# Optimization experiments

Measured on AMD Instinct MI355X. Metric: run time of the kernel, lower is better.

## Reference

```python
import jax, jax.numpy as jnp
import numpy as np
import math

CH = 96      # channels
WS = 8       # window size
SS = WS // 2 # stride
NH = 4       # heads
RED = 16     # SE reduction
B, H, W = 2, 128, 128
SCALE = (CH // NH) ** -0.5
LN_EPS = 1e-5


def setup_inputs() -> dict:
    key = jax.random.key(0)
    ks = jax.random.split(key, 16)
    def n(k, shape, s=0.02):
        return jax.random.normal(k, shape, jnp.float32) * s
    gc = CH // 3
    gcr = max(gc // RED, 1)
    return dict(
        low=jax.random.normal(ks[0], (B, CH, H, W), jnp.float32),
        high=jax.random.normal(ks[1], (B, CH, H, W), jnp.float32),
        ln1_g=jnp.ones((CH,), jnp.float32), ln1_b=jnp.zeros((CH,), jnp.float32),
        ln2_g=jnp.ones((CH,), jnp.float32), ln2_b=jnp.zeros((CH,), jnp.float32),
        se_w1=n(ks[2], (3, gcr, gc)), se_w2=n(ks[3], (3, gc, gcr)),
        wq_l=n(ks[4], (CH, CH)), wk_h=n(ks[5], (CH, CH)), wv_h=n(ks[6], (CH, CH)),
        wq_h=n(ks[7], (CH, CH)), wk_l=n(ks[8], (CH, CH)), wv_l=n(ks[9], (CH, CH)),
        wproj_l=n(ks[10], (CH, CH)), wproj_h=n(ks[11], (CH, CH)),
        mlp_w1=n(ks[12], (4 * CH, CH)), mlp_b1=jnp.zeros((4 * CH,), jnp.float32),
        mlp_w2=n(ks[13], (CH, 4 * CH)), mlp_b2=jnp.zeros((CH,), jnp.float32),
    )


def _ln(x, g, b):
    # LayerNorm over channel dim of NCHW tensor
    mu = jnp.mean(x, axis=1, keepdims=True)
    v = jnp.mean((x - mu) ** 2, axis=1, keepdims=True)
    return (x - mu) * jax.lax.rsqrt(v + LN_EPS) * g[None, :, None, None] + b[None, :, None, None]


def _win(low, high, se_w1, se_w2, wq_l, wk_h, wv_h, wq_h, wk_l, wv_l, wp_l, wp_h):
    Bz, C, Hh, Ww = low.shape
    n_h = 0 if Hh <= WS else math.ceil((Hh - WS) / SS)
    n_w = 0 if Ww <= WS else math.ceil((Ww - WS) / SS)
    Hp, Wp = n_h * SS + WS, n_w * SS + WS
    low_p = jnp.pad(low, ((0, 0), (0, 0), (0, Hp - Hh), (0, Wp - Ww)))
    high_p = jnp.pad(high, ((0, 0), (0, 0), (0, Hp - Hh), (0, Wp - Ww)))
    # SE on 3 channel groups of high
    gc = C // 3
    groups = []
    for i in range(3):
        hg = high_p[:, i * gc:(i + 1) * gc]
        pool = hg.mean((2, 3))                        # (B, gc)
        z = jax.nn.relu(pool @ se_w1[i].T)            # (B, gcr)
        s = jax.nn.sigmoid(z @ se_w2[i].T)            # (B, gc)
        groups.append(hg * s[:, :, None, None])
    high_d = jnp.concatenate(groups, axis=1)
    nHw, nWw = n_h + 1, n_w + 1
    idx_h = np.arange(nHw)[:, None] * SS + np.arange(WS)[None, :]  # (nHw, WS)
    idx_w = np.arange(nWw)[:, None] * SS + np.arange(WS)[None, :]  # (nWw, WS)

    def extract(x):  # unfold -> (B*L, C, WS*WS)
        p = x[:, :, idx_h][:, :, :, :, idx_w]          # (B,C,nHw,WS,nWw,WS)
        p = p.transpose(0, 2, 4, 1, 3, 5)              # (B,nHw,nWw,C,WS,WS)
        return p.reshape(Bz * nHw * nWw, C, WS * WS)

    lw, hw = extract(low_p), extract(high_d)
    d = C // NH

    def proj(w, x):  # 1x1 conv on flattened windows
        return jnp.einsum('oc,xcn->xon', w, x).reshape(-1, NH, d, WS * WS)

    ql, kh, vh = proj(wq_l, lw), proj(wk_h, hw), proj(wv_h, hw)
    qh, kl, vl = proj(wq_h, hw), proj(wk_l, lw), proj(wv_l, lw)
    a_lh = jax.nn.softmax(jnp.einsum('xhdn,xhdm->xhnm', ql, kh) * SCALE, axis=-1)
    a_hl = jax.nn.softmax(jnp.einsum('xhdn,xhdm->xhnm', qh, kl) * SCALE, axis=-1)
    ol = jnp.einsum('xhnm,xhdm->xhdn', a_lh, vh).reshape(Bz, nHw, nWw, C, WS, WS)
    oh = jnp.einsum('xhnm,xhdm->xhdn', a_hl, vl).reshape(Bz, nHw, nWw, C, WS, WS)
    ih = idx_h[:, :, None, None]
    iw = idx_w[None, None, :, :]

    def fold(p):  # scatter-add overlapping windows back
        p = p.transpose(0, 3, 1, 4, 2, 5)              # (B,C,nHw,WS,nWw,WS)
        return jnp.zeros((Bz, C, Hp, Wp), p.dtype).at[:, :, ih, iw].add(p)

    cnt = jnp.zeros((Hp, Wp), jnp.float32).at[ih, iw].add(jnp.ones((nHw, WS, nWw, WS), jnp.float32))
    out_l = (fold(ol) / cnt)[:, :, :Hh, :Ww]
    out_h = (fold(oh) / cnt)[:, :, :Hh, :Ww]
    return (low + jnp.einsum('oc,bchw->bohw', wp_l, out_l),
            high + jnp.einsum('oc,bchw->bohw', wp_h, out_h))


def reference(low, high, ln1_g, ln1_b, ln2_g, ln2_b, se_w1, se_w2,
              wq_l, wk_h, wv_h, wq_h, wk_l, wv_l, wproj_l, wproj_h,
              mlp_w1, mlp_b1, mlp_w2, mlp_b2):
    wargs = (se_w1, se_w2, wq_l, wk_h, wv_h, wq_h, wk_l, wv_l, wproj_l, wproj_h)
    l1 = _ln(low, ln1_g, ln1_b)
    h1 = _ln(high, ln1_g, ln1_b)
    o1_l, o1_h = _win(l1, h1, *wargs)
    low1 = low + o1_l
    high1 = high + o1_h
    s = SS
    ls = jnp.roll(low1, (-s, -s), (2, 3))
    hs = jnp.roll(high1, (-s, -s), (2, 3))
    o2_l, o2_h = _win(_ln(ls, ln2_g, ln2_b), _ln(hs, ln2_g, ln2_b), *wargs)
    low2 = low1 + jnp.roll(o2_l, (s, s), (2, 3))
    high2 = high1 + jnp.roll(o2_h, (s, s), (2, 3))

    def mlp(x):
        xf = x.transpose(0, 2, 3, 1)  # B,H,W,C
        h = jax.nn.gelu(xf @ mlp_w1.T + mlp_b1, approximate=False)
        return (h @ mlp_w2.T + mlp_b2).transpose(0, 3, 1, 2)

    return (low2 + mlp(low2), high2 + mlp(high2))
```

## Files before the change

### kernel.cpp

```cpp
#include <hip/hip_runtime.h>
#include <math.h>

#define CHN 96
#define HW 16384
#define NWIN 31
#define SCALE_F 0.20412414523193154f

typedef __attribute__((ext_vector_type(8))) __bf16 bf16x8;
typedef __attribute__((ext_vector_type(4))) float f32x4;
typedef __attribute__((ext_vector_type(8))) unsigned short u16x8;

__device__ __forceinline__ int rfl(int v) { return __builtin_amdgcn_readfirstlane(v); }

__device__ __forceinline__ unsigned short f2bf(float f) {
  union { float f; unsigned u; } v; v.f = f;
  unsigned r = v.u + 0x7fffu + ((v.u >> 16) & 1u);
  return (unsigned short)(r >> 16);
}
__device__ __forceinline__ float bf2f(unsigned short h) {
  union { unsigned u; float f; } v; v.u = ((unsigned)h) << 16;
  return v.f;
}
__device__ __forceinline__ float ldv(const float* p, size_t i) { return p[i]; }
__device__ __forceinline__ float ldv(const unsigned short* p, size_t i) { return bf2f(p[i]); }
__device__ __forceinline__ bf16x8 ld8(const unsigned short* p) {
  return *(const bf16x8*)__builtin_assume_aligned(p, 16);
}
__device__ __forceinline__ u16x8 ld8u(const unsigned short* p) {
  return *(const u16x8*)__builtin_assume_aligned(p, 16);
}
__device__ __forceinline__ bf16x8 zf8() {
  union { unsigned long long u[2]; bf16x8 v; } z;
  z.u[0] = 0ull; z.u[1] = 0ull;
  return z.v;
}
__device__ __forceinline__ void ld8f(const float* p, float* o) {
  float4 a = *(const float4*)__builtin_assume_aligned(p, 16);
  float4 b = *(const float4*)__builtin_assume_aligned(p + 4, 16);
  o[0] = a.x; o[1] = a.y; o[2] = a.z; o[3] = a.w;
  o[4] = b.x; o[5] = b.y; o[6] = b.z; o[7] = b.w;
}
__device__ __forceinline__ void ld8f(const unsigned short* p, float* o) {
  u16x8 v = ld8u(p);
#pragma unroll
  for (int u = 0; u < 8; ++u) o[u] = bf2f(v[u]);
}
__device__ __forceinline__ void ld4f(const float* p, float* o) {
  float4 a = *(const float4*)__builtin_assume_aligned(p, 16);
  o[0] = a.x; o[1] = a.y; o[2] = a.z; o[3] = a.w;
}
__device__ __forceinline__ void ld4f(const unsigned short* p, float* o) {
  ushort4 v = *(const ushort4*)__builtin_assume_aligned(p, 8);
  o[0] = bf2f(v.x); o[1] = bf2f(v.y); o[2] = bf2f(v.z); o[3] = bf2f(v.w);
}

__device__ __forceinline__ float gelu_sig(float x) {
  return x * __builtin_amdgcn_rcpf(1.f + __expf(-1.702f * x));
}

template <typename T>
__global__ __launch_bounds__(256) void ln2_k(const T* __restrict__ xl, const T* __restrict__ xh,
                                             float* __restrict__ mu_l, float* __restrict__ rs_l,
                                             float* __restrict__ mu_h, float* __restrict__ rs_h) {
  int which = blockIdx.x >> 5;
  int idx = (blockIdx.x & 31) * 256 + threadIdx.x;
  int pix0 = idx * 4;
  const T* xt = which ? xh : xl;
  float* mu = which ? mu_h : mu_l;
  float* rstd = which ? rs_h : rs_l;
  int b = pix0 >> 14, p = pix0 & 16383;
  const T* xp = xt + (size_t)b * CHN * HW + p;
  float s[4] = {0.f, 0.f, 0.f, 0.f}, s2[4] = {0.f, 0.f, 0.f, 0.f};
#pragma unroll 8
  for (int c = 0; c < CHN; ++c) {
    float v4[4];
    ld4f(xp + (size_t)c * HW, v4);
#pragma unroll
    for (int j = 0; j < 4; ++j) {
      s[j] += v4[j];
      s2[j] = fmaf(v4[j], v4[j], s2[j]);
    }
  }
  float4 mo, ro;
  float m0 = s[0] * (1.f / 96.f), m1 = s[1] * (1.f / 96.f);
  float m2 = s[2] * (1.f / 96.f), m3 = s[3] * (1.f / 96.f);
  mo.x = m0; mo.y = m1; mo.z = m2; mo.w = m3;
  ro.x = rsqrtf(fmaf(-m0, m0, s2[0] * (1.f / 96.f)) + 1e-5f);
  ro.y = rsqrtf(fmaf(-m1, m1, s2[1] * (1.f / 96.f)) + 1e-5f);
  ro.z = rsqrtf(fmaf(-m2, m2, s2[2] * (1.f / 96.f)) + 1e-5f);
  ro.w = rsqrtf(fmaf(-m3, m3, s2[3] * (1.f / 96.f)) + 1e-5f);
  *(float4*)&mu[pix0] = mo;
  *(float4*)&rstd[pix0] = ro;
}

template <typename T>
__global__ __launch_bounds__(256) void pool_k(const T* __restrict__ x,
                                              const float* __restrict__ mu,
                                              const float* __restrict__ rstd,
                                              const float* __restrict__ g,
                                              const float* __restrict__ bt,
                                              float* __restrict__ pool) {
  int blk = blockIdx.x;
  int b = blk / CHN, c = blk % CHN;
  const T* xp = x + (size_t)(b * CHN + c) * HW;
  const float* mup = mu + b * HW;
  const float* rp = rstd + b * HW;
  int t = threadIdx.x;
  float s = 0.f;
  for (int p0 = t * 4; p0 < HW; p0 += 1024) {
    float v4[4];
    ld4f(xp + p0, v4);
    float4 m4 = *(const float4*)&mup[p0];
    float4 r4 = *(const float4*)&rp[p0];
    s += (v4[0] - m4.x) * r4.x + (v4[1] - m4.y) * r4.y +
         (v4[2] - m4.z) * r4.z + (v4[3] - m4.w) * r4.w;
  }
  __shared__ float red[256];
  red[t] = s;
  __syncthreads();
  for (int k = 128; k > 0; k >>= 1) {
    if (t < k) red[t] += red[t + k];
    __syncthreads();
  }
  if (t == 0) pool[blk] = g[c] * (red[0] * (1.f / 16384.f)) + bt[c];
}

__global__ __launch_bounds__(256) void se_k(const float* __restrict__ pool,
                                            const float* __restrict__ w1,
                                            const float* __restrict__ w2,
                                            float* __restrict__ s_se) {
  int t = threadIdx.x;
  if (t >= 2 * CHN) return;
  int b = t / CHN, c = t % CHN;
  int i = c >> 5, cl = c & 31;
  const float* pg = pool + b * CHN + i * 32;
  const float* w1p = w1 + i * 64;
  float z0 = 0.f, z1 = 0.f;
#pragma unroll 8
  for (int k = 0; k < 32; ++k) {
    float p = pg[k];
    z0 = fmaf(p, w1p[k], z0);
    z1 = fmaf(p, w1p[32 + k], z1);
  }
  z0 = fmaxf(z0, 0.f);
  z1 = fmaxf(z1, 0.f);
  float a = z0 * w2[i * 64 + cl * 2] + z1 * w2[i * 64 + cl * 2 + 1];
  s_se[t] = 1.f / (1.f + __expf(-a));
}

__global__ __launch_bounds__(256) void cvt_k(const float* __restrict__ w1,
                                             const float* __restrict__ w2,
                                             const float* __restrict__ p0,
                                             const float* __restrict__ p1,
                                             const float* __restrict__ p2,
                                             const float* __restrict__ p3,
                                             const float* __restrict__ p4,
                                             const float* __restrict__ p5,
                                             const float* __restrict__ q0,
                                             const float* __restrict__ q1,
                                             unsigned short* __restrict__ w1b,
                                             unsigned short* __restrict__ w2b,
                                             unsigned short* __restrict__ wqb,
                                             unsigned short* __restrict__ wpb) {
  int i = blockIdx.x * 256 + threadIdx.x;
  if (i < 36864) {
    w1b[i] = f2bf(w1[i]);
    w2b[i] = f2bf(w2[i]);
  }
  if (i < 55296) {
    int tt = i / 9216, rem = i - tt * 9216;
    const float* ps[6] = {p0, p1, p2, p3, p4, p5};
    wqb[i] = f2bf(ps[tt][rem]);
  }
  if (i < 18432) {
    wpb[i] = f2bf(i < 9216 ? q0[i] : q1[i - 9216]);
  }
}

template <typename T>
__global__ __launch_bounds__(256, 3) void proj_k(
    const T* __restrict__ lowp, const T* __restrict__ highp,
    const float* __restrict__ mu_l, const float* __restrict__ rs_l,
    const float* __restrict__ mu_h, const float* __restrict__ rs_h,
    const float* __restrict__ g, const float* __restrict__ bt,
    const float* __restrict__ s_se,
    const unsigned short* __restrict__ wqb,
    unsigned short* __restrict__ qkv) {
  __shared__ __align__(16) unsigned short sh[13312];
  unsigned short* Xl = sh;
  unsigned short* Xh = sh + 6656;
  int t = threadIdx.x;
  int lane = t & 63;
  int w = rfl(t >> 6);
  int n16 = lane & 15, quad = lane >> 4;
  int tile = blockIdx.x;
  int Pb = tile * 64;
  int b = Pb >> 14, rr0 = Pb & 16383;

  {
    int pg = t & 7;
    float mul8[8], rsl8[8], muh8[8], rsh8[8];
    ld8f(mu_l + (size_t)b * HW + rr0 + pg * 8, mul8);
    ld8f(rs_l + (size_t)b * HW + rr0 + pg * 8, rsl8);
    ld8f(mu_h + (size_t)b * HW + rr0 + pg * 8, muh8);
    ld8f(rs_h + (size_t)b * HW + rr0 + pg * 8, rsh8);
#pragma unroll
    for (int k = 0; k < 3; ++k) {
      int c = (t + k * 256) >> 3;
      float gc = g[c], bc = bt[c], sc = s_se[b * CHN + c];
      float xl8[8], xh8[8];
      ld8f(lowp + (size_t)(b * CHN + c) * HW + rr0 + pg * 8, xl8);
      ld8f(highp + (size_t)(b * CHN + c) * HW + rr0 + pg * 8, xh8);
      int cr = c + pg * 8; if (cr >= 96) cr -= 96;
#pragma unroll
      for (int u = 0; u < 8; ++u) {
        int px = pg * 8 + u;
        Xl[px * 104 + cr] = f2bf((xl8[u] - mul8[u]) * rsl8[u] * gc + bc);
        Xh[px * 104 + cr] = f2bf(((xh8[u] - muh8[u]) * rsh8[u] * gc + bc) * sc);
      }
    }
  }
  __syncthreads();

  int tmain = (0x4310 >> (4 * w)) & 15;
  const unsigned short* Xm = (w == 0 || w == 3) ? Xl : Xh;
  const unsigned short* Xv = (w < 2) ? Xh : Xl;
  bf16x8 af[12], av[12];
  int rotb = n16 >> 3;
#pragma unroll
  for (int mi = 0; mi < 4; ++mi)
#pragma unroll
    for (int k = 0; k < 3; ++k) {
      int gidx = k * 4 + quad + 2 * mi + rotb; if (gidx >= 12) gidx -= 12;
      af[mi * 3 + k] = ld8(&Xm[(mi * 16 + n16) * 104 + gidx * 8]);
      av[mi * 3 + k] = ld8(&Xv[(mi * 16 + n16) * 104 + gidx * 8]);
    }
  __syncthreads();

  unsigned short* tw = sh + w * 3328;
#pragma unroll
  for (int half = 0; half < 2; ++half) {
#pragma unroll
    for (int ni = 0; ni < 6; ++ni) {
      f32x4 a0 = {0.f, 0.f, 0.f, 0.f}, a1 = {0.f, 0.f, 0.f, 0.f};
#pragma unroll
      for (int k = 0; k < 3; ++k) {
        bf16x8 bf = ld8(&wqb[((size_t)tmain * 96 + ni * 16 + n16) * 96 + k * 32 + quad * 8]);
        a0 = __builtin_amdgcn_mfma_f32_16x16x32_bf16(af[(half * 2 + 0) * 3 + k], bf, a0, 0, 0, 0);
        a1 = __builtin_amdgcn_mfma_f32_16x16x32_bf16(af[(half * 2 + 1) * 3 + k], bf, a1, 0, 0, 0);
      }
#pragma unroll
      for (int r = 0; r < 4; ++r) {
        tw[(quad * 4 + r) * 104 + ni * 16 + n16] = f2bf(a0[r]);
        tw[(16 + quad * 4 + r) * 104 + ni * 16 + n16] = f2bf(a1[r]);
      }
    }
#pragma unroll
    for (int c6 = 0; c6 < 6; ++c6) {
      int chunk = lane + 64 * c6;
      int pl2 = chunk / 12, kb2 = chunk - pl2 * 12;
      u16x8 v = ld8u(&tw[pl2 * 104 + kb2 * 8]);
      size_t pix = (size_t)rr0 + half * 32 + pl2;
      *(u16x8*)&qkv[((size_t)(tmain * 2 + b) * HW + pix) * 96 + kb2 * 8] = v;
    }
  }

  int tv = (w < 2) ? 2 : 5;
  int nbase = (w & 1) * 3;
#pragma unroll
  for (int jj = 0; jj < 3; ++jj) {
    int ni = nbase + jj;
    f32x4 acc[4];
#pragma unroll
    for (int mi = 0; mi < 4; ++mi) { f32x4 z = {0.f, 0.f, 0.f, 0.f}; acc[mi] = z; }
#pragma unroll
    for (int k = 0; k < 3; ++k) {
      bf16x8 bf = ld8(&wqb[((size_t)tv * 96 + ni * 16 + n16) * 96 + k * 32 + quad * 8]);
#pragma unroll
      for (int mi = 0; mi < 4; ++mi)
        acc[mi] = __builtin_amdgcn_mfma_f32_16x16x32_bf16(av[mi * 3 + k], bf, acc[mi], 0, 0, 0);
    }
    int feat = ni * 16 + n16;
    size_t rowbase = ((size_t)(tv * 2 + b) * CHN + feat) * HW + rr0;
#pragma unroll
    for (int mi = 0; mi < 4; ++mi) {
      ushort4 o4;
      o4.x = f2bf(acc[mi][0]);
      o4.y = f2bf(acc[mi][1]);
      o4.z = f2bf(acc[mi][2]);
      o4.w = f2bf(acc[mi][3]);
      *(ushort4*)&qkv[rowbase + mi * 16 + quad * 4] = o4;
    }
  }
}

__global__ __launch_bounds__(256, 4) void attn_k(
    const unsigned short* __restrict__ qkv,
    unsigned short* __restrict__ Owin, int shift) {
  __shared__ __align__(16) unsigned short shb[17152];
  unsigned short* Vs = shb;
  unsigned short* P32 = shb + 6912;
  unsigned short* Os = shb;

  int bid = blockIdx.x;
  int dir = bid / 1922;
  int rem = bid - dir * 1922;
  int b = rem / 961;
  int win = rem - b * 961;
  int wy = win / NWIN, wx = win % NWIN;
  int t = threadIdx.x;
  int lane = t & 63;
  int h = rfl(t >> 6);
  int n16 = lane & 15, quad = lane >> 4;

  {
    const unsigned short* vbase = qkv + (size_t)((dir * 3 + 2) * 2 + b) * CHN * HW;
    for (int i = t; i < 1536; i += 256) {
      int c = i >> 4, ry = (i >> 1) & 7, hx = i & 1;
      int gy = (wy * 4 + ry + shift) & 127;
      int gx = (wx * 4 + hx * 4 + shift) & 127;
      ushort4 v4 = *(const ushort4*)(vbase + (size_t)c * HW + gy * 128 + gx);
      *(ushort4*)&Vs[c * 72 + ry * 8 + hx * 4] = v4;
    }
  }

  bf16x8 qa[4], kb4[4];
  {
    const unsigned short* qpm = qkv + (size_t)((dir * 3 + 0) * 2 + b) * CHN * HW;
    const unsigned short* kpm = qkv + (size_t)((dir * 3 + 1) * 2 + b) * CHN * HW;
    if (quad < 3) {
#pragma unroll
      for (int ni = 0; ni < 4; ++ni) {
        int n = ni * 16 + n16;
        int gy = (wy * 4 + (n >> 3) + shift) & 127;
        int gx = (wx * 4 + (n & 7) + shift) & 127;
        size_t pix = (size_t)gy * 128 + gx;
        qa[ni] = ld8(&qpm[pix * 96 + h * 24 + quad * 8]);
        kb4[ni] = ld8(&kpm[pix * 96 + h * 24 + quad * 8]);
      }
    } else {
#pragma unroll
      for (int ni = 0; ni < 4; ++ni) { qa[ni] = zf8(); kb4[ni] = zf8(); }
    }
  }
  __syncthreads();

  const int hP = h * (64 * 40);

  f32x4 sa[4][4];
#pragma unroll
  for (int ni = 0; ni < 4; ++ni)
#pragma unroll
    for (int mi = 0; mi < 4; ++mi) {
      f32x4 z = {0.f, 0.f, 0.f, 0.f};
      sa[ni][mi] = __builtin_amdgcn_mfma_f32_16x16x32_bf16(qa[ni], kb4[mi], z, 0, 0, 0);
    }

#pragma unroll
  for (int ni = 0; ni < 4; ++ni)
#pragma unroll
    for (int r = 0; r < 4; ++r) {
      float e0 = __expf(sa[ni][0][r] * SCALE_F);
      float e1 = __expf(sa[ni][1][r] * SCALE_F);
      float e2 = __expf(sa[ni][2][r] * SCALE_F);
      float e3 = __expf(sa[ni][3][r] * SCALE_F);
      float sm = (e0 + e1) + (e2 + e3);
      sm += __shfl_xor(sm, 1);
      sm += __shfl_xor(sm, 2);
      sm += __shfl_xor(sm, 4);
      sm += __shfl_xor(sm, 8);
      float inv = __builtin_amdgcn_rcpf(sm);
      sa[ni][0][r] = e0 * inv;
      sa[ni][1][r] = e1 * inv;
      sa[ni][2][r] = e2 * inv;
      sa[ni][3][r] = e3 * inv;
    }

  f32x4 oa[4][2];
#pragma unroll
  for (int ni = 0; ni < 4; ++ni) {
    f32x4 z = {0.f, 0.f, 0.f, 0.f};
    oa[ni][0] = z; oa[ni][1] = z;
  }
#pragma unroll
  for (int s = 0; s < 2; ++s) {
#pragma unroll
    for (int ni = 0; ni < 4; ++ni)
#pragma unroll
      for (int r = 0; r < 4; ++r) {
#pragma unroll
        for (int mm = 0; mm < 2; ++mm) {
          int mi = s * 2 + mm;
          P32[hP + (ni * 16 + quad * 4 + r) * 40 + mm * 16 + n16] = f2bf(sa[ni][mi][r]);
        }
      }
    bf16x8 pa[4];
#pragma unroll
    for (int ni = 0; ni < 4; ++ni) pa[ni] = ld8(&P32[hP + (ni * 16 + n16) * 40 + quad * 8]);
    bf16x8 vb0 = ld8(&Vs[(h * 24 + n16) * 72 + s * 32 + quad * 8]);
    bf16x8 vb1 = (n16 < 8) ? ld8(&Vs[(h * 24 + 16 + n16) * 72 + s * 32 + quad * 8]) : zf8();
#pragma unroll
    for (int ni = 0; ni < 4; ++ni) {
      oa[ni][0] = __builtin_amdgcn_mfma_f32_16x16x32_bf16(pa[ni], vb0, oa[ni][0], 0, 0, 0);
      oa[ni][1] = __builtin_amdgcn_mfma_f32_16x16x32_bf16(pa[ni], vb1, oa[ni][1], 0, 0, 0);
    }
  }
  __syncthreads();

#pragma unroll
  for (int ni = 0; ni < 4; ++ni)
#pragma unroll
    for (int r = 0; r < 4; ++r) {
      int n = ni * 16 + quad * 4 + r;
      Os[n * 104 + h * 24 + n16] = f2bf(oa[ni][0][r]);
      if (n16 < 8) Os[n * 104 + h * 24 + 16 + n16] = f2bf(oa[ni][1][r]);
    }
  __syncthreads();

  {
    unsigned short* obase = Owin + (size_t)((dir * 2 + b) * 961 + win) * 64 * CHN;
#pragma unroll
    for (int k = 0; k < 3; ++k) {
      int i = t + k * 256;
      int px = i / 12, cb = i - px * 12;
      u16x8 v = ld8u(&Os[px * 104 + cb * 8]);
      *(u16x8*)&obase[px * CHN + cb * 8] = v;
    }
  }
}

template <typename T>
__global__ __launch_bounds__(256) void combine_k(
    const T* __restrict__ base_l, const T* __restrict__ base_h,
    unsigned short* __restrict__ out_l, unsigned short* __restrict__ out_h,
    const unsigned short* __restrict__ Owin,
    float* __restrict__ mu_lp, float* __restrict__ rs_lp,
    float* __restrict__ mu_hp, float* __restrict__ rs_hp,
    const float* __restrict__ g, const float* __restrict__ bt,
    const unsigned short* __restrict__ wpb2, int shift) {
  __shared__ __align__(16) unsigned short sb[96 * 72];
  __shared__ float red[2][4][64];
  unsigned short* at = sb;
  unsigned short* ot = sb;
  int t = threadIdx.x;
  int lane = t & 63;
  int w = rfl(t >> 6);
  int n16 = lane & 15, quad = lane >> 4;
  int sel = blockIdx.x >> 9;
  int tile = blockIdx.x & 511;
  const T* base = sel ? base_h : base_l;
  unsigned short* outp = sel ? out_h : out_l;
  float* mu = sel ? mu_hp : mu_lp;
  float* rstd = sel ? rs_hp : rs_lp;
  const unsigned short* wpb = wpb2 + sel * 9216;

#pragma unroll
  for (int k = 0; k < 3; ++k) {
    int i = t + k * 256;
    int px = i / 12, cb = i - px * 12;
    int Ps = tile * 64 + px;
    int b = Ps >> 14, rem = Ps & 16383;
    int ys = rem >> 7, xs = rem & 127;
    int wyh = ys >> 2, wxh = xs >> 2;
    float acc[8];
#pragma unroll
    for (int u = 0; u < 8; ++u) acc[u] = 0.f;
    for (int dy = 0; dy < 2; ++dy) {
      int wyc = wyh - 1 + dy;
      if ((unsigned)wyc > 30u) continue;
      int py = ys - wyc * 4;
      for (int dx = 0; dx < 2; ++dx) {
        int wxc = wxh - 1 + dx;
        if ((unsigned)wxc > 30u) continue;
        int pxl = xs - wxc * 4;
        size_t o = ((size_t)((sel * 2 + b) * 961 + wyc * 31 + wxc) * 64 + py * 8 + pxl) * CHN + cb * 8;
        u16x8 v = ld8u(&Owin[o]);
#pragma unroll
        for (int u = 0; u < 8; ++u) acc[u] += bf2f(v[u]);
      }
    }
    union { u16x8 v; unsigned short s[8]; } pk;
#pragma unroll
    for (int u = 0; u < 8; ++u) pk.s[u] = f2bf(acc[u]);
    *(u16x8*)&at[px * 104 + cb * 8] = pk.v;
  }
  __syncthreads();

  bf16x8 af[3];
#pragma unroll
  for (int k = 0; k < 3; ++k)
    af[k] = ld8(&at[(w * 16 + n16) * 104 + k * 32 + quad * 8]);

  f32x4 acc6[6];
#pragma unroll
  for (int ni = 0; ni < 6; ++ni) {
    f32x4 z = {0.f, 0.f, 0.f, 0.f};
    acc6[ni] = z;
#pragma unroll
    for (int k = 0; k < 3; ++k) {
      bf16x8 bf = ld8(&wpb[(ni * 16 + n16) * 96 + k * 32 + quad * 8]);
      acc6[ni] = __builtin_amdgcn_mfma_f32_16x16x32_bf16(af[k], bf, acc6[ni], 0, 0, 0);
    }
  }
  __syncthreads();

#pragma unroll
  for (int ni = 0; ni < 6; ++ni)
#pragma unroll
    for (int r = 0; r < 4; ++r)
      ot[(ni * 16 + n16) * 72 + w * 16 + quad * 4 + r] = f2bf(acc6[ni][r]);
  __syncthreads();

  int Ps0 = tile * 64;
  int b = Ps0 >> 14, rem0 = Ps0 & 16383;
  int ys = rem0 >> 7, xs0 = rem0 & 127;
  int yt = (ys + shift) & 127;
  float icy = (ys >= 4 && ys <= 123) ? 0.5f : 1.f;
  int px = t & 63, c0w = t >> 6;
  int xs = xs0 + px;
  int xt = (xs + shift) & 127;
  float icx = (xs >= 4 && xs <= 123) ? 0.5f : 1.f;
  float invc = icy * icx;
  int pt = b * HW + yt * 128 + xt;
  float m = mu[pt], rs = rstd[pt];
  size_t pixoff = (size_t)yt * 128 + xt;
  float s = 0.f, sq = 0.f;
#pragma unroll
  for (int k = 0; k < 24; ++k) {
    int o = c0w + 4 * k;
    size_t gidx = ((size_t)b * CHN + o) * HW + pixoff;
    float bv = ldv(base, gidx);
    float lnv = (bv - m) * rs * g[o] + bt[o];
    float v = bv + lnv + bf2f(ot[o * 72 + px]) * invc;
    outp[gidx] = f2bf(v);
    s += v;
    sq = fmaf(v, v, sq);
  }
  red[0][c0w][px] = s;
  red[1][c0w][px] = sq;
  __syncthreads();
  if (t < 64) {
    int px2 = t;
    float ss = red[0][0][px2] + red[0][1][px2] + red[0][2][px2] + red[0][3][px2];
    float qq = red[1][0][px2] + red[1][1][px2] + red[1][2][px2] + red[1][3][px2];
    int xs2 = xs0 + px2;
    int xt2 = (xs2 + shift) & 127;
    int pt2 = b * HW + yt * 128 + xt2;
    float mm = ss * (1.f / 96.f);
    float var = fmaf(-mm, mm, qq * (1.f / 96.f));
    mu[pt2] = mm;
    rstd[pt2] = rsqrtf(var + 1e-5f);
  }
}

__global__ __launch_bounds__(256, 2) void mlp_k(
    const unsigned short* __restrict__ x_l, const unsigned short* __restrict__ x_h,
    float* __restrict__ outp,
    const unsigned short* __restrict__ w1b, const float* __restrict__ b1,
    const unsigned short* __restrict__ w2b, const float* __restrict__ b2) {
  __shared__ __align__(16) unsigned char smem[51200];
  unsigned short* Xa = (unsigned short*)smem;
  unsigned short* Ha = (unsigned short*)smem;
  float* Ot = (float*)smem;

  int t = threadIdx.x;
  int lane = t & 63;
  int w = rfl(t >> 6);
  int n16 = lane & 15, quad = lane >> 4;
  int sel = blockIdx.x >> 8;
  int tile = blockIdx.x & 255;
  const unsigned short* x = sel ? x_h : x_l;
  float* op = outp + (size_t)sel * (2 * CHN * HW);
  int Pb = tile * 128;
  int b = Pb >> 14, rr0 = Pb & 16383;

  u16x8 xv6[6];
  int cc6[6], pp6[6];
#pragma unroll
  for (int k = 0; k < 6; ++k) {
    int i = t + k * 256;
    cc6[k] = i >> 4; pp6[k] = i & 15;
    xv6[k] = ld8u(&x[((size_t)b * CHN + cc6[k]) * HW + rr0 + pp6[k] * 8]);
  }
  bf16x8 wf[18];
  float b1v6[6];
#pragma unroll
  for (int h2 = 0; h2 < 2; ++h2)
#pragma unroll
    for (int ni = 0; ni < 3; ++ni) {
      int nrow = h2 * 192 + w * 48 + ni * 16 + n16;
#pragma unroll
      for (int kk = 0; kk < 3; ++kk)
        wf[(h2 * 3 + ni) * 3 + kk] = ld8(&w1b[(size_t)nrow * 96 + kk * 32 + quad * 8]);
      b1v6[h2 * 3 + ni] = b1[nrow];
    }
#pragma unroll
  for (int k = 0; k < 6; ++k) {
    int cr = cc6[k] + 8 * pp6[k];
    if (cr >= 96) cr -= 96;
    if (cr >= 96) cr -= 96;
#pragma unroll
    for (int u = 0; u < 8; ++u) Xa[(pp6[k] * 8 + u) * 104 + cr] = xv6[k][u];
  }
  __syncthreads();

  bf16x8 af[24];
  int rotb = n16 >> 3;
#pragma unroll
  for (int mi = 0; mi < 8; ++mi)
#pragma unroll
    for (int k = 0; k < 3; ++k) {
      int gidx = k * 4 + quad + 2 * mi + rotb;
      if (gidx >= 24) gidx -= 24; else if (gidx >= 12) gidx -= 12;
      af[mi * 3 + k] = ld8(&Xa[(mi * 16 + n16) * 104 + gidx * 8]);
    }
  __syncthreads();

  int ph = w & 1, fh = w >> 1;
  f32x4 acc2[4][3];
#pragma unroll
  for (int g2 = 0; g2 < 4; ++g2)
#pragma unroll
    for (int ni = 0; ni < 3; ++ni) { f32x4 z = {0.f, 0.f, 0.f, 0.f}; acc2[g2][ni] = z; }

#pragma unroll
  for (int half = 0; half < 2; ++half) {
#pragma unroll
    for (int ni = 0; ni < 3; ++ni) {
      f32x4 acc[8];
#pragma unroll
      for (int mi = 0; mi < 8; ++mi) { f32x4 z = {0.f, 0.f, 0.f, 0.f}; acc[mi] = z; }
#pragma unroll
      for (int kk = 0; kk < 3; ++kk) {
        bf16x8 bf = wf[(half * 3 + ni) * 3 + kk];
#pragma unroll
        for (int mi = 0; mi < 8; ++mi)
          acc[mi] = __builtin_amdgcn_mfma_f32_16x16x32_bf16(af[mi * 3 + kk], bf, acc[mi], 0, 0, 0);
      }
      int fl = w * 48 + ni * 16 + n16;
      float b1v = b1v6[half * 3 + ni];
#pragma unroll
      for (int mi = 0; mi < 8; ++mi)
#pragma unroll
        for (int r = 0; r < 4; ++r)
          Ha[(mi * 16 + quad * 4 + r) * 200 + fl] = f2bf(gelu_sig(acc[mi][r] + b1v));
    }
    __syncthreads();

#pragma unroll
    for (int kc = 0; kc < 2; ++kc) {
      bf16x8 w2f[9];
#pragma unroll
      for (int kk = 0; kk < 3; ++kk)
#pragma unroll
        for (int ni = 0; ni < 3; ++ni)
          w2f[kk * 3 + ni] = ld8(&w2b[((size_t)(fh * 48 + ni * 16 + n16)) * 384 +
                                      half * 192 + (kc * 3 + kk) * 32 + quad * 8]);
#pragma unroll
      for (int kk = 0; kk < 3; ++kk) {
        int k0 = kc * 3 + kk;
        bf16x8 a2[4];
#pragma unroll
        for (int g2 = 0; g2 < 4; ++g2)
          a2[g2] = ld8(&Ha[((ph * 4 + g2) * 16 + n16) * 200 + k0 * 32 + quad * 8]);
#pragma unroll
        for (int ni = 0; ni < 3; ++ni)
#pragma unroll
          for (int g2 = 0; g2 < 4; ++g2)
            acc2[g2][ni] = __builtin_amdgcn_mfma_f32_16x16x32_bf16(a2[g2], w2f[kk * 3 + ni], acc2[g2][ni], 0, 0, 0);
      }
    }
    __syncthreads();
  }

#pragma unroll
  for (int g2 = 0; g2 < 4; ++g2)
#pragma unroll
    for (int ni = 0; ni < 3; ++ni)
#pragma unroll
      for (int r = 0; r < 4; ++r)
        Ot[(fh * 48 + ni * 16 + n16) * 132 + (ph * 4 + g2) * 16 + quad * 4 + r] = acc2[g2][ni][r];
  __syncthreads();

#pragma unroll
  for (int k = 0; k < 12; ++k) {
    int i = t + k * 256;
    int o = i >> 5, pg = i & 31;
    size_t gbase = ((size_t)b * CHN + o) * HW + rr0 + pg * 4;
    ushort4 xv = *(const ushort4*)&x[gbase];
    float4 ov = *(const float4*)&Ot[o * 132 + pg * 4];
    float bb = b2[o];
    float4 res;
    res.x = bf2f(xv.x) + ov.x + bb;
    res.y = bf2f(xv.y) + ov.y + bb;
    res.z = bf2f(xv.z) + ov.z + bb;
    res.w = bf2f(xv.w) + ov.w + bb;
    *(float4*)&op[gbase] = res;
  }
}

extern "C" void kernel_launch(void* const* d_in, const int* in_sizes, int n_in,
                              void* d_out, int out_size, void* d_ws, size_t ws_size,
                              hipStream_t stream) {
  (void)in_sizes; (void)n_in; (void)out_size; (void)ws_size;
  const float* low   = (const float*)d_in[0];
  const float* high  = (const float*)d_in[1];
  const float* ln1_g = (const float*)d_in[2];
  const float* ln1_b = (const float*)d_in[3];
  const float* ln2_g = (const float*)d_in[4];
  const float* ln2_b = (const float*)d_in[5];
  const float* se_w1 = (const float*)d_in[6];
  const float* se_w2 = (const float*)d_in[7];
  const float* wq_l  = (const float*)d_in[8];
  const float* wk_h  = (const float*)d_in[9];
  const float* wv_h  = (const float*)d_in[10];
  const float* wq_h  = (const float*)d_in[11];
  const float* wk_l  = (const float*)d_in[12];
  const float* wv_l  = (const float*)d_in[13];
  const float* wp_l  = (const float*)d_in[14];
  const float* wp_h  = (const float*)d_in[15];
  const float* mw1   = (const float*)d_in[16];
  const float* mb1   = (const float*)d_in[17];
  const float* mw2   = (const float*)d_in[18];
  const float* mb2   = (const float*)d_in[19];

  float* ws = (float*)d_ws;
  unsigned short* w1b = (unsigned short*)ws;
  unsigned short* w2b = w1b + 36864;
  unsigned short* wqb = w2b + 36864;
  unsigned short* wpb = wqb + 55296;
  float* mu_l  = ws + 73728;
  float* rs_l  = mu_l + 32768;
  float* mu_h  = rs_l + 32768;
  float* rs_h  = mu_h + 32768;
  float* poolb = rs_h + 32768;
  float* s_se  = poolb + 256;
  unsigned short* low1b  = (unsigned short*)(s_se + 256);
  unsigned short* high1b = low1b + 3145728;
  unsigned short* qkv    = high1b + 3145728;
  unsigned short* Owin   = qkv + 18874368;

  cvt_k<<<216, 256, 0, stream>>>(mw1, mw2, wq_l, wk_h, wv_h, wq_h, wk_l, wv_l,
                                 wp_l, wp_h, w1b, w2b, wqb, wpb);

  ln2_k<float><<<64, 256, 0, stream>>>(low, high, mu_l, rs_l, mu_h, rs_h);

  for (int pass = 0; pass < 2; ++pass) {
    const float* g  = pass ? ln2_g : ln1_g;
    const float* bt = pass ? ln2_b : ln1_b;
    int shift = pass ? 4 : 0;

    if (pass == 0) {
      pool_k<float><<<192, 256, 0, stream>>>(high, mu_h, rs_h, g, bt, poolb);
      se_k<<<1, 256, 0, stream>>>(poolb, se_w1, se_w2, s_se);
      proj_k<float><<<512, 256, 0, stream>>>(low, high, mu_l, rs_l, mu_h, rs_h,
                                             g, bt, s_se, wqb, qkv);
      attn_k<<<2 * 1922, 256, 0, stream>>>(qkv, Owin, shift);
      combine_k<float><<<1024, 256, 0, stream>>>(low, high, low1b, high1b, Owin,
                                                 mu_l, rs_l, mu_h, rs_h,
                                                 g, bt, wpb, shift);
    } else {
      pool_k<unsigned short><<<192, 256, 0, stream>>>(high1b, mu_h, rs_h, g, bt, poolb);
      se_k<<<1, 256, 0, stream>>>(poolb, se_w1, se_w2, s_se);
      proj_k<unsigned short><<<512, 256, 0, stream>>>(low1b, high1b, mu_l, rs_l, mu_h, rs_h,
                                                      g, bt, s_se, wqb, qkv);
      attn_k<<<2 * 1922, 256, 0, stream>>>(qkv, Owin, shift);
      combine_k<unsigned short><<<1024, 256, 0, stream>>>(low1b, high1b, low1b, high1b, Owin,
                                                          mu_l, rs_l, mu_h, rs_h,
                                                          g, bt, wpb, shift);
    }
  }
  mlp_k<<<512, 256, 0, stream>>>(low1b, high1b, (float*)d_out, w1b, mb1, w2b, mb2);
}
```

Measured before the change: 335.7 us.

## Defer softmax normalization via MFMA row-sum and shrink P LDS stride

Replaces the per-row softmax shuffle reductions with exp2 of pre-scaled scores, then computes row sums with an extra MFMA against a ones vector and normalizes the PV output afterwards. The P staging buffer stride drops from 40 to 36, which shrinks shared memory so launch bounds can raise occupancy to 5 blocks per CU. This removes the cross-lane shuffles and per-element multiplies but adds MFMA work. The row sum now comes from bf16-rounded probabilities, which slightly changes numerics, and the new stride may change LDS bank conflicts.

```diff
diff --git a/kernel.cpp b/kernel.cpp
--- a/kernel.cpp
+++ b/kernel.cpp
@@ -5,6 +5,7 @@
 #define HW 16384
 #define NWIN 31
 #define SCALE_F 0.20412414523193154f
+#define SCALE_L2 0.294488893f
 
 typedef __attribute__((ext_vector_type(8))) __bf16 bf16x8;
 typedef __attribute__((ext_vector_type(4))) float f32x4;
@@ -21,6 +22,13 @@
   union { unsigned u; float f; } v; v.u = ((unsigned)h) << 16;
   return v.f;
 }
+__device__ __forceinline__ float fexp2(float x) {
+#if __has_builtin(__builtin_amdgcn_exp2f)
+  return __builtin_amdgcn_exp2f(x);
+#else
+  return __expf(x * 0.6931471806f);
+#endif
+}
 __device__ __forceinline__ float ldv(const float* p, size_t i) { return p[i]; }
 __device__ __forceinline__ float ldv(const unsigned short* p, size_t i) { return bf2f(p[i]); }
 __device__ __forceinline__ bf16x8 ld8(const unsigned short* p) {
@@ -33,6 +41,12 @@
   union { unsigned long long u[2]; bf16x8 v; } z;
   z.u[0] = 0ull; z.u[1] = 0ull;
   return z.v;
+}
+__device__ __forceinline__ bf16x8 onesf8() {
+  union { unsigned short s[8]; bf16x8 v; } o;
+#pragma unroll
+  for (int i = 0; i < 8; ++i) o.s[i] = 0x3F80;
+  return o.v;
 }
 __device__ __forceinline__ void ld8f(const float* p, float* o) {
   float4 a = *(const float4*)__builtin_assume_aligned(p, 16);
@@ -294,10 +308,10 @@
   }
 }
 
-__global__ __launch_bounds__(256, 4) void attn_k(
+__global__ __launch_bounds__(256, 5) void attn_k(
     const unsigned short* __restrict__ qkv,
     unsigned short* __restrict__ Owin, int shift) {
-  __shared__ __align__(16) unsigned short shb[17152];
+  __shared__ __align__(16) unsigned short shb[16128];
   unsigned short* Vs = shb;
   unsigned short* P32 = shb + 6912;
   unsigned short* Os = shb;
@@ -345,7 +359,7 @@
   }
   __syncthreads();
 
-  const int hP = h * (64 * 40);
+  const int hP = h * (64 * 36);
 
   f32x4 sa[4][4];
 #pragma unroll
@@ -359,28 +373,18 @@
 #pragma unroll
   for (int ni = 0; ni < 4; ++ni)
 #pragma unroll
-    for (int r = 0; r < 4; ++r) {
-      float e0 = __expf(sa[ni][0][r] * SCALE_F);
-      float e1 = __expf(sa[ni][1][r] * SCALE_F);
-      float e2 = __expf(sa[ni][2][r] * SCALE_F);
-      float e3 = __expf(sa[ni][3][r] * SCALE_F);
-      float sm = (e0 + e1) + (e2 + e3);
-      sm += __shfl_xor(sm, 1);
-      sm += __shfl_xor(sm, 2);
-      sm += __shfl_xor(sm, 4);
-      sm += __shfl_xor(sm, 8);
-      float inv = __builtin_amdgcn_rcpf(sm);
-      sa[ni][0][r] = e0 * inv;
-      sa[ni][1][r] = e1 * inv;
-      sa[ni][2][r] = e2 * inv;
-      sa[ni][3][r] = e3 * inv;
-    }
-
+    for (int mi = 0; mi < 4; ++mi)
+#pragma unroll
+      for (int r = 0; r < 4; ++r)
+        sa[ni][mi][r] = fexp2(sa[ni][mi][r] * SCALE_L2);
+
+  const bf16x8 ones = onesf8();
   f32x4 oa[4][2];
+  f32x4 sacc[4];
 #pragma unroll
   for (int ni = 0; ni < 4; ++ni) {
     f32x4 z = {0.f, 0.f, 0.f, 0.f};
-    oa[ni][0] = z; oa[ni][1] = z;
+    oa[ni][0] = z; oa[ni][1] = z; sacc[ni] = z;
   }
 #pragma unroll
   for (int s = 0; s < 2; ++s) {
@@ -391,20 +395,30 @@
 #pragma unroll
         for (int mm = 0; mm < 2; ++mm) {
           int mi = s * 2 + mm;
-          P32[hP + (ni * 16 + quad * 4 + r) * 40 + mm * 16 + n16] = f2bf(sa[ni][mi][r]);
+          P32[hP + (ni * 16 + quad * 4 + r) * 36 + mm * 16 + n16] = f2bf(sa[ni][mi][r]);
         }
       }
     bf16x8 pa[4];
 #pragma unroll
-    for (int ni = 0; ni < 4; ++ni) pa[ni] = ld8(&P32[hP + (ni * 16 + n16) * 40 + quad * 8]);
+    for (int ni = 0; ni < 4; ++ni) pa[ni] = ld8(&P32[hP + (ni * 16 + n16) * 36 + quad * 8]);
     bf16x8 vb0 = ld8(&Vs[(h * 24 + n16) * 72 + s * 32 + quad * 8]);
     bf16x8 vb1 = (n16 < 8) ? ld8(&Vs[(h * 24 + 16 + n16) * 72 + s * 32 + quad * 8]) : zf8();
 #pragma unroll
     for (int ni = 0; ni < 4; ++ni) {
       oa[ni][0] = __builtin_amdgcn_mfma_f32_16x16x32_bf16(pa[ni], vb0, oa[ni][0], 0, 0, 0);
       oa[ni][1] = __builtin_amdgcn_mfma_f32_16x16x32_bf16(pa[ni], vb1, oa[ni][1], 0, 0, 0);
-    }
-  }
+      sacc[ni] = __builtin_amdgcn_mfma_f32_16x16x32_bf16(pa[ni], ones, sacc[ni], 0, 0, 0);
+    }
+  }
+
+#pragma unroll
+  for (int ni = 0; ni < 4; ++ni)
+#pragma unroll
+    for (int r = 0; r < 4; ++r) {
+      float inv = __builtin_amdgcn_rcpf(sacc[ni][r]);
+      oa[ni][0][r] *= inv;
+      oa[ni][1][r] *= inv;
+    }
   __syncthreads();
 
 #pragma unroll
```

Result: no change. 340.6 us (+1.5%).
